# Optimization experiments

Measured on AMD Instinct MI355X. Metric: run time of the kernel, lower is better.

## Reference

```python
import jax, jax.numpy as jnp
import numpy as np

N, IN_DIM, OUT_DIM, H = 1024, 128, 128, 4
D = OUT_DIM // H  # head_dim = 32
NEG_SLOPE = 0.2
MASK_VAL = -1e9
LN_EPS = 1e-5


def setup_inputs() -> dict:
    key = jax.random.key(0)
    k = jax.random.split(key, 8)
    h = jax.random.normal(k[0], (N, IN_DIM), dtype=jnp.float32)
    adj = jax.random.randint(k[1], (N, N), 0, 2, dtype=jnp.int32)
    adj = adj.at[jnp.arange(N), jnp.arange(N)].set(1)  # self-loops
    s = 1.0 / np.sqrt(IN_DIM)
    W_l = jax.random.normal(k[2], (IN_DIM, OUT_DIM), dtype=jnp.float32) * s
    W_r = jax.random.normal(k[3], (IN_DIM, OUT_DIM), dtype=jnp.float32) * s
    W_v = jax.random.normal(k[4], (IN_DIM, OUT_DIM), dtype=jnp.float32) * s
    a = jax.random.normal(k[5], (D,), dtype=jnp.float32) * (1.0 / np.sqrt(D))
    ln_g = jnp.ones((OUT_DIM,), dtype=jnp.float32)
    ln_b = jnp.zeros((OUT_DIM,), dtype=jnp.float32)
    return {"h": h, "adj": adj, "W_l": W_l, "W_r": W_r, "W_v": W_v,
            "a": a, "ln_g": ln_g, "ln_b": ln_b}


def reference(h, adj, W_l, W_r, W_v, a, ln_g, ln_b):
    n = h.shape[0]
    Wlh = (h @ W_l).reshape(n, H, D)   # [N,H,D]
    Wrh = (h @ W_r).reshape(n, H, D)   # [N,H,D]
    # pairwise additive scores: pair[i,j,h,d] = Wlh[i] + Wrh[j]
    pair = Wlh[:, None, :, :] + Wrh[None, :, :, :]          # [N,N,H,D]
    pair = jnp.where(pair >= 0, pair, NEG_SLOPE * pair)      # leaky_relu(0.2)
    e = jnp.einsum('ijhd,d->ijh', pair, a)                   # [N,N,H]
    mask = (adj != 0)[:, :, None]                            # [N,N,1]
    e = jnp.where(mask, e, MASK_VAL)
    alpha = jax.nn.softmax(e, axis=1)                        # softmax over j
    v = (h @ W_v).reshape(n, H, D)                           # [N,H,D]
    agg = jnp.einsum('ijh,jhd->ihd', alpha, v).reshape(n, OUT_DIM)
    mu = jnp.mean(agg, axis=-1, keepdims=True)
    var = jnp.mean((agg - mu) ** 2, axis=-1, keepdims=True)
    y = (agg - mu) * jax.lax.rsqrt(var + LN_EPS) * ln_g + ln_b
    return jax.nn.relu(y)
```

## Files before the change

### kernel.cpp

```cpp
#include <hip/hip_runtime.h>
#include <cstdint>

typedef _Float16 f16;
typedef _Float16 f16x2 __attribute__((ext_vector_type(2)));
typedef _Float16 f16x4 __attribute__((ext_vector_type(4)));
typedef _Float16 f16x8 __attribute__((ext_vector_type(8)));
typedef float    f32x4 __attribute__((ext_vector_type(4)));
typedef unsigned short u16;
typedef unsigned int   u32;

#define LOG2E 1.44269504088896340736f

__device__ __forceinline__ f16x2 habs2(f16x2 v) {
    union { f16x2 h; u32 u; } x; x.h = v; x.u &= 0x7FFF7FFFu; return x.h;
}
#if __has_builtin(__builtin_amdgcn_fdot2)
__device__ __forceinline__ float fdot2f(f16x2 a, f16x2 b, float c) {
    return __builtin_amdgcn_fdot2(a, b, c, false);
}
#else
__device__ __forceinline__ float fdot2f(f16x2 a, f16x2 b, float c) {
    return c + (float)a.x * (float)b.x + (float)a.y * (float)b.y;
}
#endif
#if __has_builtin(__builtin_amdgcn_exp2f)
#define EXP2F __builtin_amdgcn_exp2f
#else
#define EXP2F exp2f
#endif

__global__ __launch_bounds__(64) void k0_prep(
        const float* __restrict__ Wl, const float* __restrict__ Wr,
        const float* __restrict__ Wv, const float* __restrict__ h,
        f16* __restrict__ WT, f16* __restrict__ h16) {
    int b = blockIdx.x, t = threadIdx.x;
    if (b < 384) {
        int w = b >> 7, o = b & 127;
        const float* W = (w == 0) ? Wl : ((w == 1) ? Wr : Wv);
        f16* dst = WT + (w * 128 + o) * 128;
        #pragma unroll
        for (int kk = 0; kk < 2; kk++) {
            int k = t + kk * 64;
            dst[k] = (f16)W[k * 128 + o];
        }
    } else {
        int r0 = (b - 384) * 8;
        const float* src = h + r0 * 128;
        f16* dst = h16 + r0 * 128;
        int base = t * 16;
        #pragma unroll
        for (int e = 0; e < 16; e++) dst[base + e] = (f16)src[base + e];
    }
}

__global__ __launch_bounds__(384) void k1_proj(
        const f16* __restrict__ WT, const f16* __restrict__ h16,
        f16* __restrict__ Wlh, f16* __restrict__ WrL, f16* __restrict__ VL) {
    int t = threadIdx.x;
    int i0 = blockIdx.x * 4;
    int wsel = t >> 7, col = t & 127;

    f16x2 w2[64];
    {
        const f16x2* src = (const f16x2*)(WT + t * 128);
        #pragma unroll
        for (int c2 = 0; c2 < 64; c2++) w2[c2] = src[c2];
    }
    #pragma unroll
    for (int i = 0; i < 4; i++) {
        int j = i0 + i;
        const f16x2* hr = (const f16x2*)(h16 + j * 128);
        float acc = 0.f;
        #pragma unroll
        for (int c2 = 0; c2 < 64; c2++) acc = fdot2f(hr[c2], w2[c2], acc);
        f16 hv = (f16)acc;
        if (wsel == 0) {
            Wlh[j * 128 + col] = hv;
        } else if (wsel == 1) {
            int hh = col >> 5, dd = col & 31, c = dd >> 2, l = dd & 3;
            WrL[((hh * 8 + c) * 1024 + j) * 4 + l] = hv;
        } else {
            int hh = col >> 5, dd = col & 31;
            VL[(hh * 32 + dd) * 1024 + j] = hv;
        }
    }
}

__global__ __launch_bounds__(512) void GATv2Layer_84447646974220_kernel(
        const f16* __restrict__ Wlh, const f16* __restrict__ WrL,
        const f16* __restrict__ VL,  const int* __restrict__ adj,
        const float* __restrict__ a_, const float* __restrict__ ln_g,
        const float* __restrict__ ln_b, float* __restrict__ out) {

    __shared__ __align__(16) f16 ep[4][4][1024];
    __shared__ float aggS[2][4][128];
    __shared__ float redM[2][4][4];
    __shared__ float redS[2][4][4];

    const int t    = threadIdx.x;
    const int w    = t >> 6;
    const int lane = t & 63;
    const int hh   = w & 3;
    const int half = w >> 2;
    const int i0   = blockIdx.x * 4;

    f16x2 p2[16], q2[16];
    #pragma unroll
    for (int d2 = 0; d2 < 16; d2++) {
        float a0 = a_[2 * d2], a1 = a_[2 * d2 + 1];
        f16x2 p; p.x = (f16)(0.6f * a0); p.y = (f16)(0.6f * a1);
        f16x2 q; q.x = (f16)(0.4f * a0); q.y = (f16)(0.4f * a1);
        p2[d2] = p; q2[d2] = q;
    }
    f16x2 wl2[4][16];
    #pragma unroll
    for (int ii = 0; ii < 4; ii++) {
        const f16x2* src = (const f16x2*)(Wlh + (i0 + ii) * 128 + hh * 32);
        #pragma unroll
        for (int c2 = 0; c2 < 16; c2++) wl2[ii][c2] = src[c2];
    }

    float maxE[4];
    #pragma unroll
    for (int ii = 0; ii < 4; ii++) maxE[ii] = -__builtin_inff();

    #pragma unroll 1
    for (int jb = 0; jb < 8; jb++) {
        int j = half * 512 + jb * 64 + lane;
        f16x4 wr[8];
        #pragma unroll
        for (int c = 0; c < 8; c++)
            wr[c] = *(const f16x4*)(WrL + ((hh * 8 + c) * 1024 + j) * 4);
        int am[4];
        #pragma unroll
        for (int ii = 0; ii < 4; ii++) am[ii] = adj[(i0 + ii) * 1024 + j];

        float e[4] = {0.f, 0.f, 0.f, 0.f};
        #pragma unroll
        for (int c = 0; c < 8; c++) {
            #pragma unroll
            for (int ii = 0; ii < 4; ii++) {
                f16x2 t0 = wl2[ii][2 * c]     + wr[c].lo;
                f16x2 t1 = wl2[ii][2 * c + 1] + wr[c].hi;
                e[ii] = fdot2f(p2[2 * c],     t0, e[ii]);
                e[ii] = fdot2f(q2[2 * c],     habs2(t0), e[ii]);
                e[ii] = fdot2f(p2[2 * c + 1], t1, e[ii]);
                e[ii] = fdot2f(q2[2 * c + 1], habs2(t1), e[ii]);
            }
        }
        #pragma unroll
        for (int ii = 0; ii < 4; ii++) {
            float v = am[ii] ? e[ii] : -__builtin_inff();
            maxE[ii] = fmaxf(maxE[ii], v);
            ep[hh][ii][j] = (f16)v;
        }
    }

    #pragma unroll
    for (int ii = 0; ii < 4; ii++) {
        float M = maxE[ii];
        #pragma unroll
        for (int off = 32; off > 0; off >>= 1) M = fmaxf(M, __shfl_xor(M, off));
        if (lane == 0) redM[half][hh][ii] = M;
    }
    __syncthreads();

    #pragma unroll
    for (int ii = 0; ii < 4; ii++) {
        float M = fmaxf(redM[0][hh][ii], redM[1][hh][ii]);
        f16x8 v0 = *(f16x8*)&ep[hh][ii][half * 512 + lane * 8];
        float pb[8], l = 0.f;
        #pragma unroll
        for (int e = 0; e < 8; e++) pb[e] = EXP2F(((float)v0[e] - M) * LOG2E);
        #pragma unroll
        for (int e = 0; e < 8; e++) { v0[e] = (f16)pb[e]; l += pb[e]; }
        *(f16x8*)&ep[hh][ii][half * 512 + lane * 8] = v0;
        #pragma unroll
        for (int off = 32; off > 0; off >>= 1) l += __shfl_xor(l, off);
        if (lane == 0) redS[half][hh][ii] = l;
    }
    __syncthreads();

    float lr[4];
    #pragma unroll
    for (int ii = 0; ii < 4; ii++)
        lr[ii] = 1.0f / (redS[0][hh][ii] + redS[1][hh][ii]);

    f32x4 acc0 = {0.f, 0.f, 0.f, 0.f}, acc1 = {0.f, 0.f, 0.f, 0.f};
    const int q8  = (lane >> 4) << 3;
    const int m3  = lane & 3;
    const int n15 = lane & 15;

    #pragma unroll 1
    for (int jt4 = 0; jt4 < 4; jt4++) {
        int jt = half * 4 + jt4;
        #pragma unroll
        for (int kk = 0; kk < 4; kk++) {
            int ko = jt * 128 + kk * 32 + q8;
            f16x8 af = *(const f16x8*)&ep[hh][m3][ko];
            f16x8 b0 = *(const f16x8*)(VL + (hh * 32 + n15) * 1024 + ko);
            f16x8 b1 = *(const f16x8*)(VL + (hh * 32 + 16 + n15) * 1024 + ko);
            acc0 = __builtin_amdgcn_mfma_f32_16x16x32_f16(af, b0, acc0, 0, 0, 0);
            acc1 = __builtin_amdgcn_mfma_f32_16x16x32_f16(af, b1, acc1, 0, 0, 0);
        }
    }

    if (lane < 16) {
        #pragma unroll
        for (int r = 0; r < 4; r++) {
            aggS[half][r][hh * 32 + lane]      = acc0[r] * lr[r];
            aggS[half][r][hh * 32 + 16 + lane] = acc1[r] * lr[r];
        }
    }
    __syncthreads();

    if (w < 4) {
        float x0 = aggS[0][w][lane]      + aggS[1][w][lane];
        float x1 = aggS[0][w][lane + 64] + aggS[1][w][lane + 64];
        float s = x0 + x1, sq = x0 * x0 + x1 * x1;
        #pragma unroll
        for (int off = 32; off > 0; off >>= 1) {
            s  += __shfl_xor(s, off);
            sq += __shfl_xor(sq, off);
        }
        float mean = s * (1.f / 128.f);
        float var  = sq * (1.f / 128.f) - mean * mean;
        float rs   = rsqrtf(var + 1e-5f);
        float y0 = fmaxf((x0 - mean) * rs * ln_g[lane]      + ln_b[lane],      0.f);
        float y1 = fmaxf((x1 - mean) * rs * ln_g[lane + 64] + ln_b[lane + 64], 0.f);
        out[(i0 + w) * 128 + lane]      = y0;
        out[(i0 + w) * 128 + 64 + lane] = y1;
    }
}

extern "C" void kernel_launch(void* const* d_in, const int* in_sizes, int n_in,
                              void* d_out, int out_size, void* d_ws, size_t ws_size,
                              hipStream_t stream) {
    const float* h   = (const float*)d_in[0];
    const int*   adj = (const int*)d_in[1];
    const float* Wl  = (const float*)d_in[2];
    const float* Wr  = (const float*)d_in[3];
    const float* Wv  = (const float*)d_in[4];
    const float* a_  = (const float*)d_in[5];
    const float* g_  = (const float*)d_in[6];
    const float* b_  = (const float*)d_in[7];
    float* out = (float*)d_out;

    char* ws = (char*)d_ws;
    f16* WT  = (f16*)(ws);
    f16* h16 = (f16*)(ws + 98304);
    f16* Wlh = (f16*)(ws + 360448);
    f16* WrL = (f16*)(ws + 622592);
    f16* VL  = (f16*)(ws + 884736);

    k0_prep<<<512, 64, 0, stream>>>(Wl, Wr, Wv, h, WT, h16);
    k1_proj<<<256, 384, 0, stream>>>(WT, h16, Wlh, WrL, VL);
    GATv2Layer_84447646974220_kernel<<<256, 512, 0, stream>>>(
        Wlh, WrL, VL, adj, a_, g_, b_, out);
}
```

Before: 99.13 us.

## Split leaky-relu dot into linear per-node terms and fuse prep into projection

Rewrites leaky_relu(x)·a as 0.6·a·x + 0.4·a·|x|. The linear part separates into per-node scalars AL[i] and BR[j], which the projection kernel computes with a wavefront shuffle reduction. This halves the fdot2 work in the O(N²) score loop. It also drops the separate prep kernel by converting the weights and h to fp16 inside the projection kernel, removing one launch at the cost of strided fp32 weight reads per block.

```diff
diff --git a/kernel.cpp b/kernel.cpp
--- a/kernel.cpp
+++ b/kernel.cpp
@@ -29,59 +29,57 @@
 #define EXP2F exp2f
 #endif
 
-__global__ __launch_bounds__(64) void k0_prep(
+__global__ __launch_bounds__(384) void k1_proj(
         const float* __restrict__ Wl, const float* __restrict__ Wr,
         const float* __restrict__ Wv, const float* __restrict__ h,
-        f16* __restrict__ WT, f16* __restrict__ h16) {
-    int b = blockIdx.x, t = threadIdx.x;
-    if (b < 384) {
-        int w = b >> 7, o = b & 127;
-        const float* W = (w == 0) ? Wl : ((w == 1) ? Wr : Wv);
-        f16* dst = WT + (w * 128 + o) * 128;
-        #pragma unroll
-        for (int kk = 0; kk < 2; kk++) {
-            int k = t + kk * 64;
-            dst[k] = (f16)W[k * 128 + o];
-        }
-    } else {
-        int r0 = (b - 384) * 8;
-        const float* src = h + r0 * 128;
-        f16* dst = h16 + r0 * 128;
-        int base = t * 16;
-        #pragma unroll
-        for (int e = 0; e < 16; e++) dst[base + e] = (f16)src[base + e];
-    }
-}
-
-__global__ __launch_bounds__(384) void k1_proj(
-        const f16* __restrict__ WT, const f16* __restrict__ h16,
-        f16* __restrict__ Wlh, f16* __restrict__ WrL, f16* __restrict__ VL) {
-    int t = threadIdx.x;
-    int i0 = blockIdx.x * 4;
-    int wsel = t >> 7, col = t & 127;
-
+        const float* __restrict__ a_,
+        f16* __restrict__ Wlh, f16* __restrict__ WrL, f16* __restrict__ VL,
+        float* __restrict__ AL, float* __restrict__ BR) {
+    __shared__ __align__(16) f16 hS[4][128];
+    const int t    = threadIdx.x;
+    const int i0   = blockIdx.x * 4;
+    const int wsel = t >> 7, col = t & 127;
+    const int lane = t & 63;
+
+    for (int e = t; e < 512; e += 384)
+        ((f16*)hS)[e] = (f16)h[i0 * 128 + e];
+
+    const float* W = (wsel == 0) ? Wl : ((wsel == 1) ? Wr : Wv);
     f16x2 w2[64];
-    {
-        const f16x2* src = (const f16x2*)(WT + t * 128);
-        #pragma unroll
-        for (int c2 = 0; c2 < 64; c2++) w2[c2] = src[c2];
-    }
+    #pragma unroll
+    for (int c2 = 0; c2 < 64; c2++) {
+        f16x2 v;
+        v.x = (f16)W[(2 * c2) * 128 + col];
+        v.y = (f16)W[(2 * c2 + 1) * 128 + col];
+        w2[c2] = v;
+    }
+    const float asc = 0.6f * a_[col & 31];
+    __syncthreads();
+
     #pragma unroll
     for (int i = 0; i < 4; i++) {
-        int j = i0 + i;
-        const f16x2* hr = (const f16x2*)(h16 + j * 128);
+        const int j = i0 + i;
+        const f16x2* hr = (const f16x2*)hS[i];
         float acc = 0.f;
         #pragma unroll
         for (int c2 = 0; c2 < 64; c2++) acc = fdot2f(hr[c2], w2[c2], acc);
-        f16 hv = (f16)acc;
+        const f16 hv = (f16)acc;
+        const int hh = col >> 5, dd = col & 31;
         if (wsel == 0) {
             Wlh[j * 128 + col] = hv;
         } else if (wsel == 1) {
-            int hh = col >> 5, dd = col & 31, c = dd >> 2, l = dd & 3;
-            WrL[((hh * 8 + c) * 1024 + j) * 4 + l] = hv;
+            WrL[((hh * 8 + (dd >> 2)) * 1024 + j) * 4 + (dd & 3)] = hv;
         } else {
-            int hh = col >> 5, dd = col & 31;
             VL[(hh * 32 + dd) * 1024 + j] = hv;
+        }
+        if (wsel < 2) {
+            float part = asc * acc;
+            #pragma unroll
+            for (int off = 1; off < 32; off <<= 1) part += __shfl_xor(part, off);
+            if ((lane & 31) == 0) {
+                if (wsel == 0) AL[j * 4 + hh] = part;
+                else           BR[hh * 1024 + j] = part;
+            }
         }
     }
 }
@@ -89,6 +87,7 @@
 __global__ __launch_bounds__(512) void GATv2Layer_84447646974220_kernel(
         const f16* __restrict__ Wlh, const f16* __restrict__ WrL,
         const f16* __restrict__ VL,  const int* __restrict__ adj,
+        const float* __restrict__ AL, const float* __restrict__ BR,
         const float* __restrict__ a_, const float* __restrict__ ln_g,
         const float* __restrict__ ln_b, float* __restrict__ out) {
 
@@ -104,20 +103,20 @@
     const int half = w >> 2;
     const int i0   = blockIdx.x * 4;
 
-    f16x2 p2[16], q2[16];
+    f16x2 q2[16];
     #pragma unroll
     for (int d2 = 0; d2 < 16; d2++) {
-        float a0 = a_[2 * d2], a1 = a_[2 * d2 + 1];
-        f16x2 p; p.x = (f16)(0.6f * a0); p.y = (f16)(0.6f * a1);
-        f16x2 q; q.x = (f16)(0.4f * a0); q.y = (f16)(0.4f * a1);
-        p2[d2] = p; q2[d2] = q;
+        f16x2 q; q.x = (f16)(0.4f * a_[2 * d2]); q.y = (f16)(0.4f * a_[2 * d2 + 1]);
+        q2[d2] = q;
     }
     f16x2 wl2[4][16];
+    float al[4];
     #pragma unroll
     for (int ii = 0; ii < 4; ii++) {
         const f16x2* src = (const f16x2*)(Wlh + (i0 + ii) * 128 + hh * 32);
         #pragma unroll
         for (int c2 = 0; c2 < 16; c2++) wl2[ii][c2] = src[c2];
+        al[ii] = AL[(i0 + ii) * 4 + hh];
     }
 
     float maxE[4];
@@ -134,23 +133,24 @@
         int am[4];
         #pragma unroll
         for (int ii = 0; ii < 4; ii++) am[ii] = adj[(i0 + ii) * 1024 + j];
-
-        float e[4] = {0.f, 0.f, 0.f, 0.f};
+        float bj = BR[hh * 1024 + j];
+
+        float e[4];
+        #pragma unroll
+        for (int ii = 0; ii < 4; ii++) e[ii] = al[ii];
         #pragma unroll
         for (int c = 0; c < 8; c++) {
             #pragma unroll
             for (int ii = 0; ii < 4; ii++) {
                 f16x2 t0 = wl2[ii][2 * c]     + wr[c].lo;
                 f16x2 t1 = wl2[ii][2 * c + 1] + wr[c].hi;
-                e[ii] = fdot2f(p2[2 * c],     t0, e[ii]);
                 e[ii] = fdot2f(q2[2 * c],     habs2(t0), e[ii]);
-                e[ii] = fdot2f(p2[2 * c + 1], t1, e[ii]);
                 e[ii] = fdot2f(q2[2 * c + 1], habs2(t1), e[ii]);
             }
         }
         #pragma unroll
         for (int ii = 0; ii < 4; ii++) {
-            float v = am[ii] ? e[ii] : -__builtin_inff();
+            float v = am[ii] ? (e[ii] + bj) : -__builtin_inff();
             maxE[ii] = fmaxf(maxE[ii], v);
             ep[hh][ii][j] = (f16)v;
         }
@@ -247,14 +247,13 @@
     float* out = (float*)d_out;
 
     char* ws = (char*)d_ws;
-    f16* WT  = (f16*)(ws);
-    f16* h16 = (f16*)(ws + 98304);
-    f16* Wlh = (f16*)(ws + 360448);
-    f16* WrL = (f16*)(ws + 622592);
-    f16* VL  = (f16*)(ws + 884736);
-
-    k0_prep<<<512, 64, 0, stream>>>(Wl, Wr, Wv, h, WT, h16);
-    k1_proj<<<256, 384, 0, stream>>>(WT, h16, Wlh, WrL, VL);
+    f16*   Wlh = (f16*)(ws);
+    f16*   WrL = (f16*)(ws + 262144);
+    f16*   VL  = (f16*)(ws + 524288);
+    float* AL  = (float*)(ws + 786432);
+    float* BR  = (float*)(ws + 802816);
+
+    k1_proj<<<256, 384, 0, stream>>>(Wl, Wr, Wv, h, a_, Wlh, WrL, VL, AL, BR);
     GATv2Layer_84447646974220_kernel<<<256, 512, 0, stream>>>(
-        Wlh, WrL, VL, adj, a_, g_, b_, out);
-}
+        Wlh, WrL, VL, adj, AL, BR, a_, g_, b_, out);
+}
```

After: 96.25 us. 1.03x faster.
